# Performance work log

Measured on AMD Instinct MI355X. Metric: run time of the kernel, lower is better.

Reference implementation:

```python
import jax, jax.numpy as jnp
import numpy as np

# Layer config (matches init_kwargs)
K0, K1 = 4, 4   # kernel_size
S0, S1 = 2, 2   # strides


def setup_inputs() -> dict:
    key = jax.random.key(0)
    # [batch, width, height, depth] as read in the original call()
    inputs = jax.random.normal(key, (16, 112, 112, 128), dtype=jnp.float32)
    return {"inputs": inputs}


def _patch_indices(size, k, s):
    # ceil-division count of strides, as in -((size - k) // -s) + 1
    n = -((size - k) // -s) + 1
    # for each patch start i*s, take [i*s, i*s+1, ..., i*s+k-1]
    idx = (jnp.arange(n)[:, None] * s + jnp.arange(k)[None, :]).reshape(-1)
    return n, idx  # idx shape: (n*k,)


def reference(inputs):
    B, W, H, D = inputs.shape
    nh, ih = _patch_indices(W, K0, S0)  # horizontal over axis 1 (width)
    nv, iv = _patch_indices(H, K1, S1)  # vertical over axis 2 (height)
    # double gather, mirroring tf.gather(tf.gather(x, ih, 1), iv, 2)
    g = jnp.take(inputs, ih, axis=1)          # [B, nh*K0, H, D]
    g = jnp.take(g, iv, axis=2)               # [B, nh*K0, nv*K1, D]
    # [B, nh, K0, nv, K1, D] -> perm [0,1,3,2,4,5] -> [B, nh, nv, K0, K1, D]
    g = g.reshape(B, nh, K0, nv, K1, D).transpose(0, 1, 3, 2, 4, 5)
    # flatten patches: [B, nh*nv, K0*K1*D]
    return g.reshape(B, nh * nv, K0 * K1 * D)
```

## Files before the change

kernel.cpp:

```cpp
#include <hip/hip_runtime.h>


typedef float f32x4 __attribute__((ext_vector_type(4)));

#define NH 55
#define NV 55
#define W_IN 112
#define H_IN 112
#define D4 32
#define PPB 8

__global__ __launch_bounds__(512) void patch_copy_kernel(
    const float* __restrict__ in, float* __restrict__ out) {
    const int base = blockIdx.x * PPB;

    const int tid = threadIdx.x;
    const int d4 = tid & 31;
    const int k1 = (tid >> 5) & 3;
    const int k0 = tid >> 7;

    const f32x4* __restrict__ src4 = reinterpret_cast<const f32x4*>(in);
    f32x4* __restrict__ dst4 = reinterpret_cast<f32x4*>(out);

    f32x4 v[PPB];

    #pragma unroll
    for (int p = 0; p < PPB; ++p) {
        const int blk = base + p;
        const int pv = blk % NV;
        const int t1 = blk / NV;
        const int ph = t1 % NH;
        const int b  = t1 / NH;
        const int w = ph * 2 + k0;
        const int h = pv * 2 + k1;
        v[p] = src4[(size_t)((b * W_IN + w) * H_IN + h) * D4 + d4];
    }

    #pragma unroll
    for (int p = 0; p < PPB; ++p) {
        const int blk = base + p;
        __builtin_nontemporal_store(v[p], &dst4[(size_t)blk * 512 + tid]);
    }
}

extern "C" void kernel_launch(void* const* d_in, const int* in_sizes, int n_in,
                              void* d_out, int out_size, void* d_ws, size_t ws_size,
                              hipStream_t stream) {
    const float* in = (const float*)d_in[0];
    float* out = (float*)d_out;

    const int nblocks = 16 * NH * NV / PPB;
    patch_copy_kernel<<<nblocks, 512, 0, stream>>>(in, out);
}
```

Measured before the change: 94.34 us.

## Replace gather-per-output with scatter-per-input so each input row is read once

The kernel is restructured from one thread per output element gathering from the input to one block per input (batch, width) row, where each thread loads a float4 and writes it to every patch position (up to four) that contains it. This removes the roughly fourfold redundant input reads of the gather form. The cost is scattered, predicated store patterns with less contiguous writes per wavefront, and only 1792 blocks of 512 threads, which may hurt store coalescing and occupancy.

```diff
diff --git a/kernel.cpp b/kernel.cpp
--- a/kernel.cpp
+++ b/kernel.cpp
@@ -3,43 +3,63 @@
 
 typedef float f32x4 __attribute__((ext_vector_type(4)));
 
+#define W_IN 112
+#define H_IN 112
 #define NH 55
 #define NV 55
-#define W_IN 112
-#define H_IN 112
 #define D4 32
-#define PPB 8
+#define ITERS 7
 
-__global__ __launch_bounds__(512) void patch_copy_kernel(
+__global__ __launch_bounds__(512) void scatter_kernel(
     const float* __restrict__ in, float* __restrict__ out) {
-    const int base = blockIdx.x * PPB;
-
+    const int blk = blockIdx.x;
+    const int w = blk % W_IN;
+    const int b = blk / W_IN;
     const int tid = threadIdx.x;
     const int d4 = tid & 31;
-    const int k1 = (tid >> 5) & 3;
-    const int k0 = tid >> 7;
+    const int dh = tid >> 5;
+
+    const int k0a = w & 1;
+    const int pha = (w - k0a) >> 1;
+    const int k0b = k0a + 2;
+    const int phb = pha - 1;
+    const bool vA = (pha < NH);
+    const bool vB = (phb >= 0);
+    const int pha_c = vA ? pha : 0;
+    const int phb_c = vB ? phb : 0;
 
     const f32x4* __restrict__ src4 = reinterpret_cast<const f32x4*>(in);
     f32x4* __restrict__ dst4 = reinterpret_cast<f32x4*>(out);
 
-    f32x4 v[PPB];
+    f32x4 v[ITERS];
+    #pragma unroll
+    for (int it = 0; it < ITERS; ++it) {
+        const int h = it * 16 + dh;
+        v[it] = src4[(size_t)(blk * H_IN + h) * D4 + d4];
+    }
+
+    const size_t baseA = (size_t)(b * (NH * NV) + pha_c * NV) * 512 + (size_t)(k0a * 128) + d4;
+    const size_t baseB = (size_t)(b * (NH * NV) + phb_c * NV) * 512 + (size_t)(k0b * 128) + d4;
 
     #pragma unroll
-    for (int p = 0; p < PPB; ++p) {
-        const int blk = base + p;
-        const int pv = blk % NV;
-        const int t1 = blk / NV;
-        const int ph = t1 % NH;
-        const int b  = t1 / NH;
-        const int w = ph * 2 + k0;
-        const int h = pv * 2 + k1;
-        v[p] = src4[(size_t)((b * W_IN + w) * H_IN + h) * D4 + d4];
-    }
-
-    #pragma unroll
-    for (int p = 0; p < PPB; ++p) {
-        const int blk = base + p;
-        __builtin_nontemporal_store(v[p], &dst4[(size_t)blk * 512 + tid]);
+    for (int it = 0; it < ITERS; ++it) {
+        const int h = it * 16 + dh;
+        const int k1a = h & 1;
+        const int pva = (h - k1a) >> 1;
+        const int pvb = pva - 1;
+        const int k1b = k1a + 2;
+        const bool vC = (pva < NV);
+        const bool vD = (pvb >= 0);
+        const size_t offC = (size_t)(vC ? pva : 0) * 512 + (size_t)(k1a * 32);
+        const size_t offD = (size_t)(vD ? pvb : 0) * 512 + (size_t)(k1b * 32);
+        if (vA) {
+            if (vC) __builtin_nontemporal_store(v[it], &dst4[baseA + offC]);
+            if (vD) __builtin_nontemporal_store(v[it], &dst4[baseA + offD]);
+        }
+        if (vB) {
+            if (vC) __builtin_nontemporal_store(v[it], &dst4[baseB + offC]);
+            if (vD) __builtin_nontemporal_store(v[it], &dst4[baseB + offD]);
+        }
     }
 }
 
@@ -49,6 +69,6 @@
     const float* in = (const float*)d_in[0];
     float* out = (float*)d_out;
 
-    const int nblocks = 16 * NH * NV / PPB;
-    patch_copy_kernel<<<nblocks, 512, 0, stream>>>(in, out);
+    const int nblocks = 16 * W_IN;
+    scatter_kernel<<<nblocks, 512, 0, stream>>>(in, out);
 }
```

Result: faster. 86.16 us, median of 2 (-8.7%).
